# Optimization experiments

Measured on AMD Instinct MI355X. Metric: run time of the kernel, lower is better.

Reference implementation:

```python
import jax, jax.numpy as jnp
import numpy as np

# Dims: L list entries, T hutch samples, D = output_dim*inducing_size, H = 16 hidden
L, T, D, H = 32, 64, 8192, 16


def setup_inputs() -> dict:
    key = jax.random.key(0)
    k = jax.random.split(key, 4)
    return {
        "u": jax.random.normal(k[0], (L, D), jnp.float32),
        "w": jax.random.normal(k[1], (L, T, D), jnp.float32),  # Hutchinson Gaussian probes
        "W1": jax.random.normal(k[2], (H, D), jnp.float32) / np.sqrt(D).astype(np.float32),
        "b1": jnp.zeros((H,), jnp.float32),
        "W2": jax.random.normal(k[3], (D, H), jnp.float32) / np.sqrt(H).astype(np.float32),
        "b2": jnp.zeros((D,), jnp.float32),
    }


def reference(u, w, W1, b1, W2, b2):
    # f = W2 tanh(W1 u + b1) + b2 ; Jacobian J = W2 diag(1 - h^2) W1
    h = jnp.tanh(u @ W1.T + b1)                 # [L, H]
    f = h @ W2.T + b2                           # [L, D]  (f_u_list stacked)
    s = 1.0 - h * h                             # tanh' at preactivation, [L, H]
    # u_grad = J^T w  computed without materializing J: W1^T diag(s) W2^T w
    v = jnp.einsum('ltd,dh->lth', w, W2)        # W2^T w, [L, T, H]
    v = v * s[:, None, :]                       # diag(s) applied
    g = jnp.einsum('lth,hd->ltd', v, W1)        # J^T w, [L, T, D]
    traces = jnp.sum(g * w, axis=-1)            # w^T J w, [L, T]
    # mean over hutch samples, then mean over list entries -> [1, 1] like torch.mm output
    trace_final_mean = jnp.mean(traces).reshape(1, 1)
    return f, trace_final_mean
```

## Files before the change

### kernel.cpp

```cpp
#include <hip/hip_runtime.h>

typedef __attribute__((ext_vector_type(8))) short bf16x8;
typedef __attribute__((ext_vector_type(4))) float f32x4;

namespace {
constexpr int L = 32, T = 64, D = 8192, H = 16;
constexpr int M = L * T;
constexpr int KP = 16;
constexpr int CHUNK = D / KP;

constexpr size_t WS_WH  = 0;
constexpr size_t WS_WL  = WS_WH + 32 * 8192 / 2;
constexpr size_t WS_PRE = WS_WL + 32 * 8192 / 2;
constexpr size_t WS_AC  = WS_PRE + 32 * 8 * 16;
}

__device__ inline void split1(float f, short& h, short& l) {
  unsigned b = __float_as_uint(f);
  h = (short)(b >> 16);
  float lf = f - __uint_as_float(b & 0xFFFF0000u);
  l = (short)(__float_as_uint(lf) >> 16);
}

__device__ inline void split8(float4 a0, float4 a1, bf16x8& h, bf16x8& l) {
  float f[8] = {a0.x, a0.y, a0.z, a0.w, a1.x, a1.y, a1.z, a1.w};
#pragma unroll
  for (int i = 0; i < 8; ++i) {
    short hh, ll;
    split1(f[i], hh, ll);
    h[i] = hh; l[i] = ll;
  }
}

__global__ void k_prep_wcat(const float* __restrict__ W1,
                            const float* __restrict__ W2,
                            ushort* __restrict__ wh, ushort* __restrict__ wl,
                            float* __restrict__ ac, float* __restrict__ out) {
  int b = blockIdx.x, tid = threadIdx.x;
  if (b == 0 && tid == 0) out[(size_t)L * D] = 0.f;
  if (b < 32) {
    int d = b * 256 + tid;
    const float4* src = reinterpret_cast<const float4*>(W2 + (size_t)d * 16);
    float4 q0 = src[0], q1 = src[1], q2 = src[2], q3 = src[3];
    float v[16] = {q0.x, q0.y, q0.z, q0.w, q1.x, q1.y, q1.z, q1.w,
                   q2.x, q2.y, q2.z, q2.w, q3.x, q3.y, q3.z, q3.w};
#pragma unroll
    for (int c = 0; c < 16; ++c) {
      short hh, ll;
      split1(v[c], hh, ll);
      wh[(size_t)c * D + d] = (ushort)hh;
      wl[(size_t)c * D + d] = (ushort)ll;
    }
  } else if (b < 64) {
    int q = (b - 32) * 256 + tid;
#pragma unroll
    for (int j = 0; j < 4; ++j) {
      int idx = (q + j * 8192) * 4;
      float4 qv = *reinterpret_cast<const float4*>(W1 + idx);
      short h0, l0, h1, l1, h2, l2, h3, l3;
      split1(qv.x, h0, l0); split1(qv.y, h1, l1);
      split1(qv.z, h2, l2); split1(qv.w, h3, l3);
      ushort4 vh = {(ushort)h0, (ushort)h1, (ushort)h2, (ushort)h3};
      ushort4 vl = {(ushort)l0, (ushort)l1, (ushort)l2, (ushort)l3};
      *reinterpret_cast<ushort4*>(wh + (size_t)16 * D + idx) = vh;
      *reinterpret_cast<ushort4*>(wl + (size_t)16 * D + idx) = vl;
    }
  } else {
    int t = (b - 64) * 256 + tid;
    float4 z = {0.f, 0.f, 0.f, 0.f};
    float4* dst = reinterpret_cast<float4*>(ac);
#pragma unroll
    for (int j = 0; j < 4; ++j) dst[t + j * 4096] = z;
  }
}

__global__ void k_preact(const float* __restrict__ u,
                         const float* __restrict__ W1,
                         float* __restrict__ pre_partial) {
  int kc = blockIdx.x, l = blockIdx.y, tid = threadIdx.x;
  int d = kc * 1024 + tid * 4;
  float4 uv = *reinterpret_cast<const float4*>(u + (size_t)l * D + d);
  float acc[16];
#pragma unroll
  for (int h = 0; h < 16; ++h) {
    float4 wv = *reinterpret_cast<const float4*>(W1 + (size_t)h * D + d);
    float t = fmaf(uv.x, wv.x, 0.f);
    t = fmaf(uv.y, wv.y, t);
    t = fmaf(uv.z, wv.z, t);
    acc[h] = fmaf(uv.w, wv.w, t);
  }
#pragma unroll
  for (int h = 0; h < 16; ++h)
    for (int off = 1; off < 64; off <<= 1) acc[h] += __shfl_xor(acc[h], off);
  __shared__ float red[4][16];
  int lane = tid & 63, wv_ = tid >> 6;
  if (lane == 0) {
#pragma unroll
    for (int h = 0; h < 16; ++h) red[wv_][h] = acc[h];
  }
  __syncthreads();
  if (tid < 16)
    pre_partial[((size_t)l * 8 + kc) * 16 + tid] =
        red[0][tid] + red[1][tid] + red[2][tid] + red[3][tid];
}

__global__ void k_f(const float* __restrict__ pre_partial,
                    const float* __restrict__ b1,
                    const float* __restrict__ W2,
                    const float* __restrict__ b2,
                    float* __restrict__ fout) {
  __shared__ float hl[8][16];
  int tid = threadIdx.x;
  int lg = blockIdx.y;
  if (tid < 128) {
    int ll = tid >> 4, h = tid & 15, l = lg * 8 + ll;
    float p = b1[h];
#pragma unroll
    for (int kc = 0; kc < 8; ++kc) p += pre_partial[((size_t)l * 8 + kc) * 16 + h];
    hl[ll][h] = tanhf(p);
  }
  __syncthreads();
  int d = blockIdx.x * 256 + tid;
  const float4* w2r = reinterpret_cast<const float4*>(W2 + (size_t)d * 16);
  float4 q0 = w2r[0], q1 = w2r[1], q2 = w2r[2], q3 = w2r[3];
  float w2v[16] = {q0.x, q0.y, q0.z, q0.w, q1.x, q1.y, q1.z, q1.w,
                   q2.x, q2.y, q2.z, q2.w, q3.x, q3.y, q3.z, q3.w};
  float bv = b2[d];
#pragma unroll
  for (int ll = 0; ll < 8; ++ll) {
    float fv = bv;
#pragma unroll
    for (int h = 0; h < 16; ++h) fv = fmaf(hl[ll][h], w2v[h], fv);
    fout[(size_t)(lg * 8 + ll) * D + d] = fv;
  }
}

__global__ __launch_bounds__(256) void k_trace_ac(
    const float* __restrict__ w,
    const ushort* __restrict__ wh, const ushort* __restrict__ wl,
    float* __restrict__ ac) {
  int tid = threadIdx.x;
  int wave = tid >> 6, lane = tid & 63;
  int lrow = lane & 15, kg = lane >> 4;
  int kp = blockIdx.x;
  int rt = blockIdx.y * 4 + wave;
  int m0 = rt * 16;
  int k0 = kp * CHUNK;

  const float*  wrow = w  + (size_t)(m0 + lrow) * D + k0 + kg * 8;
  const ushort* bh0  = wh + (size_t)lrow * D + k0 + kg * 8;
  const ushort* bl0  = wl + (size_t)lrow * D + k0 + kg * 8;
  const ushort* bh1  = bh0 + (size_t)16 * D;
  const ushort* bl1  = bl0 + (size_t)16 * D;

  f32x4 acc0 = {0.f, 0.f, 0.f, 0.f};
  f32x4 acc1 = {0.f, 0.f, 0.f, 0.f};

  for (int kk = 0; kk < CHUNK / 32; ++kk) {
    int off = kk * 32;
    float4 a0 = *reinterpret_cast<const float4*>(wrow + off);
    float4 a1 = *reinterpret_cast<const float4*>(wrow + off + 4);
    bf16x8 ah, al;
    split8(a0, a1, ah, al);
    bf16x8 vbh0 = *reinterpret_cast<const bf16x8*>(bh0 + off);
    bf16x8 vbl0 = *reinterpret_cast<const bf16x8*>(bl0 + off);
    bf16x8 vbh1 = *reinterpret_cast<const bf16x8*>(bh1 + off);
    bf16x8 vbl1 = *reinterpret_cast<const bf16x8*>(bl1 + off);
    acc0 = __builtin_amdgcn_mfma_f32_16x16x32_bf16(ah, vbh0, acc0, 0, 0, 0);
    acc0 = __builtin_amdgcn_mfma_f32_16x16x32_bf16(ah, vbl0, acc0, 0, 0, 0);
    acc0 = __builtin_amdgcn_mfma_f32_16x16x32_bf16(al, vbh0, acc0, 0, 0, 0);
    acc1 = __builtin_amdgcn_mfma_f32_16x16x32_bf16(ah, vbh1, acc1, 0, 0, 0);
    acc1 = __builtin_amdgcn_mfma_f32_16x16x32_bf16(ah, vbl1, acc1, 0, 0, 0);
    acc1 = __builtin_amdgcn_mfma_f32_16x16x32_bf16(al, vbh1, acc1, 0, 0, 0);
  }

  float* dst = ac + (size_t)(m0 + kg * 4) * 32;
#pragma unroll
  for (int j = 0; j < 4; ++j) {
    atomicAdd(dst + (size_t)j * 32 + lrow,      acc0[j]);
    atomicAdd(dst + (size_t)j * 32 + 16 + lrow, acc1[j]);
  }
}

__global__ void k_trace_red(const float* __restrict__ ac,
                            const float* __restrict__ pre_partial,
                            const float* __restrict__ b1,
                            float* __restrict__ out) {
  __shared__ float s[16];
  int tid = threadIdx.x;
  int l = blockIdx.x;
  int m = l * 64 + tid;
  if (tid < 16) {
    float p = b1[tid];
#pragma unroll
    for (int kc = 0; kc < 8; ++kc) p += pre_partial[((size_t)l * 8 + kc) * 16 + tid];
    float t = tanhf(p);
    s[tid] = 1.f - t * t;
  }
  __syncthreads();
  const float4* src = reinterpret_cast<const float4*>(ac + (size_t)m * 32);
  float av[16], cv[16];
#pragma unroll
  for (int j = 0; j < 4; ++j) {
    float4 q = src[j];
    av[j * 4 + 0] = q.x; av[j * 4 + 1] = q.y;
    av[j * 4 + 2] = q.z; av[j * 4 + 3] = q.w;
  }
#pragma unroll
  for (int j = 0; j < 4; ++j) {
    float4 q = src[4 + j];
    cv[j * 4 + 0] = q.x; cv[j * 4 + 1] = q.y;
    cv[j * 4 + 2] = q.z; cv[j * 4 + 3] = q.w;
  }
  float tr = 0.f;
#pragma unroll
  for (int h = 0; h < 16; ++h) tr = fmaf(s[h] * av[h], cv[h], tr);
  for (int off = 1; off < 64; off <<= 1) tr += __shfl_xor(tr, off);
  if (tid == 0) atomicAdd(out + (size_t)L * D, tr * (1.0f / (float)(L * T)));
}

extern "C" void kernel_launch(void* const* d_in, const int* in_sizes, int n_in,
                              void* d_out, int out_size, void* d_ws, size_t ws_size,
                              hipStream_t stream) {
  const float* u  = (const float*)d_in[0];
  const float* w  = (const float*)d_in[1];
  const float* W1 = (const float*)d_in[2];
  const float* b1 = (const float*)d_in[3];
  const float* W2 = (const float*)d_in[4];
  const float* b2 = (const float*)d_in[5];
  float* out = (float*)d_out;
  float* ws  = (float*)d_ws;
  ushort* wcat_h = (ushort*)(ws + WS_WH);
  ushort* wcat_l = (ushort*)(ws + WS_WL);
  float* pre = ws + WS_PRE;
  float* acb = ws + WS_AC;

  hipLaunchKernelGGL(k_prep_wcat, dim3(80), dim3(256), 0, stream, W1, W2, wcat_h, wcat_l, acb, out);
  hipLaunchKernelGGL(k_preact,    dim3(8, 32), dim3(256), 0, stream, u, W1, pre);
  hipLaunchKernelGGL(k_f,         dim3(32, 4), dim3(256), 0, stream, pre, b1, W2, b2, out);
  hipLaunchKernelGGL(k_trace_ac,  dim3(KP, 32), dim3(256), 0, stream, w, wcat_h, wcat_l, acb);
  hipLaunchKernelGGL(k_trace_red, dim3(32), dim3(64), 0, stream, acb, pre, b1, out);
}
```

Measured before the change: 132.4 us.

## Merge five launches into three and double K-split of trace kernel

Folds the preactivation partials into the weight-prep kernel and merges the f computation with the trace reduction into a single tail kernel, cutting the launch count from five to three. The trace MFMA kernel now splits K into 32 chunks instead of 16 and its inner loop is fully unrolled, giving twice as many blocks to hide memory latency. In exchange there are twice as many atomic adds into the accumulator buffer. The f output is now computed after the trace kernel rather than before it.

```diff
diff --git a/kernel.cpp b/kernel.cpp
--- a/kernel.cpp
+++ b/kernel.cpp
@@ -6,7 +6,7 @@
 namespace {
 constexpr int L = 32, T = 64, D = 8192, H = 16;
 constexpr int M = L * T;
-constexpr int KP = 16;
+constexpr int KP = 32;
 constexpr int CHUNK = D / KP;
 
 constexpr size_t WS_WH  = 0;
@@ -32,10 +32,12 @@
   }
 }
 
-__global__ void k_prep_wcat(const float* __restrict__ W1,
-                            const float* __restrict__ W2,
-                            ushort* __restrict__ wh, ushort* __restrict__ wl,
-                            float* __restrict__ ac, float* __restrict__ out) {
+__global__ __launch_bounds__(256) void k_setup(
+    const float* __restrict__ u, const float* __restrict__ W1,
+    const float* __restrict__ W2,
+    ushort* __restrict__ wh, ushort* __restrict__ wl,
+    float* __restrict__ pre, float* __restrict__ ac,
+    float* __restrict__ out) {
   int b = blockIdx.x, tid = threadIdx.x;
   if (b == 0 && tid == 0) out[(size_t)L * D] = 0.f;
   if (b < 32) {
@@ -65,73 +67,39 @@
       *reinterpret_cast<ushort4*>(wh + (size_t)16 * D + idx) = vh;
       *reinterpret_cast<ushort4*>(wl + (size_t)16 * D + idx) = vl;
     }
-  } else {
+  } else if (b < 80) {
     int t = (b - 64) * 256 + tid;
     float4 z = {0.f, 0.f, 0.f, 0.f};
     float4* dst = reinterpret_cast<float4*>(ac);
 #pragma unroll
     for (int j = 0; j < 4; ++j) dst[t + j * 4096] = z;
-  }
-}
-
-__global__ void k_preact(const float* __restrict__ u,
-                         const float* __restrict__ W1,
-                         float* __restrict__ pre_partial) {
-  int kc = blockIdx.x, l = blockIdx.y, tid = threadIdx.x;
-  int d = kc * 1024 + tid * 4;
-  float4 uv = *reinterpret_cast<const float4*>(u + (size_t)l * D + d);
-  float acc[16];
-#pragma unroll
-  for (int h = 0; h < 16; ++h) {
-    float4 wv = *reinterpret_cast<const float4*>(W1 + (size_t)h * D + d);
-    float t = fmaf(uv.x, wv.x, 0.f);
-    t = fmaf(uv.y, wv.y, t);
-    t = fmaf(uv.z, wv.z, t);
-    acc[h] = fmaf(uv.w, wv.w, t);
-  }
-#pragma unroll
-  for (int h = 0; h < 16; ++h)
-    for (int off = 1; off < 64; off <<= 1) acc[h] += __shfl_xor(acc[h], off);
-  __shared__ float red[4][16];
-  int lane = tid & 63, wv_ = tid >> 6;
-  if (lane == 0) {
-#pragma unroll
-    for (int h = 0; h < 16; ++h) red[wv_][h] = acc[h];
-  }
-  __syncthreads();
-  if (tid < 16)
-    pre_partial[((size_t)l * 8 + kc) * 16 + tid] =
-        red[0][tid] + red[1][tid] + red[2][tid] + red[3][tid];
-}
-
-__global__ void k_f(const float* __restrict__ pre_partial,
-                    const float* __restrict__ b1,
-                    const float* __restrict__ W2,
-                    const float* __restrict__ b2,
-                    float* __restrict__ fout) {
-  __shared__ float hl[8][16];
-  int tid = threadIdx.x;
-  int lg = blockIdx.y;
-  if (tid < 128) {
-    int ll = tid >> 4, h = tid & 15, l = lg * 8 + ll;
-    float p = b1[h];
-#pragma unroll
-    for (int kc = 0; kc < 8; ++kc) p += pre_partial[((size_t)l * 8 + kc) * 16 + h];
-    hl[ll][h] = tanhf(p);
-  }
-  __syncthreads();
-  int d = blockIdx.x * 256 + tid;
-  const float4* w2r = reinterpret_cast<const float4*>(W2 + (size_t)d * 16);
-  float4 q0 = w2r[0], q1 = w2r[1], q2 = w2r[2], q3 = w2r[3];
-  float w2v[16] = {q0.x, q0.y, q0.z, q0.w, q1.x, q1.y, q1.z, q1.w,
-                   q2.x, q2.y, q2.z, q2.w, q3.x, q3.y, q3.z, q3.w};
-  float bv = b2[d];
-#pragma unroll
-  for (int ll = 0; ll < 8; ++ll) {
-    float fv = bv;
-#pragma unroll
-    for (int h = 0; h < 16; ++h) fv = fmaf(hl[ll][h], w2v[h], fv);
-    fout[(size_t)(lg * 8 + ll) * D + d] = fv;
+  } else {
+    int bb = b - 80;
+    int kc = bb & 7, l = bb >> 3;
+    int d = kc * 1024 + tid * 4;
+    float4 uv = *reinterpret_cast<const float4*>(u + (size_t)l * D + d);
+    float acc[16];
+#pragma unroll
+    for (int h = 0; h < 16; ++h) {
+      float4 wv = *reinterpret_cast<const float4*>(W1 + (size_t)h * D + d);
+      float t = fmaf(uv.x, wv.x, 0.f);
+      t = fmaf(uv.y, wv.y, t);
+      t = fmaf(uv.z, wv.z, t);
+      acc[h] = fmaf(uv.w, wv.w, t);
+    }
+#pragma unroll
+    for (int h = 0; h < 16; ++h)
+      for (int off = 1; off < 64; off <<= 1) acc[h] += __shfl_xor(acc[h], off);
+    __shared__ float red[4][16];
+    int lane = tid & 63, wv_ = tid >> 6;
+    if (lane == 0) {
+#pragma unroll
+      for (int h = 0; h < 16; ++h) red[wv_][h] = acc[h];
+    }
+    __syncthreads();
+    if (tid < 16)
+      pre[((size_t)l * 8 + kc) * 16 + tid] =
+          red[0][tid] + red[1][tid] + red[2][tid] + red[3][tid];
   }
 }
 
@@ -156,6 +124,7 @@
   f32x4 acc0 = {0.f, 0.f, 0.f, 0.f};
   f32x4 acc1 = {0.f, 0.f, 0.f, 0.f};
 
+#pragma unroll
   for (int kk = 0; kk < CHUNK / 32; ++kk) {
     int off = kk * 32;
     float4 a0 = *reinterpret_cast<const float4*>(wrow + off);
@@ -182,41 +151,69 @@
   }
 }
 
-__global__ void k_trace_red(const float* __restrict__ ac,
-                            const float* __restrict__ pre_partial,
-                            const float* __restrict__ b1,
-                            float* __restrict__ out) {
-  __shared__ float s[16];
-  int tid = threadIdx.x;
-  int l = blockIdx.x;
-  int m = l * 64 + tid;
-  if (tid < 16) {
-    float p = b1[tid];
-#pragma unroll
-    for (int kc = 0; kc < 8; ++kc) p += pre_partial[((size_t)l * 8 + kc) * 16 + tid];
-    float t = tanhf(p);
-    s[tid] = 1.f - t * t;
+__global__ __launch_bounds__(256) void k_tail(
+    const float* __restrict__ pre, const float* __restrict__ b1,
+    const float* __restrict__ W2, const float* __restrict__ b2,
+    const float* __restrict__ ac, float* __restrict__ out) {
+  int b = blockIdx.x, tid = threadIdx.x;
+  if (b >= 128) {
+    __shared__ float s[16];
+    int l = b - 128;
+    if (tid < 16) {
+      float p = b1[tid];
+#pragma unroll
+      for (int kc = 0; kc < 8; ++kc) p += pre[((size_t)l * 8 + kc) * 16 + tid];
+      float t = tanhf(p);
+      s[tid] = 1.f - t * t;
+    }
+    __syncthreads();
+    if (tid < 64) {
+      int m = l * 64 + tid;
+      const float4* src = reinterpret_cast<const float4*>(ac + (size_t)m * 32);
+      float av[16], cv[16];
+#pragma unroll
+      for (int j = 0; j < 4; ++j) {
+        float4 q = src[j];
+        av[j * 4 + 0] = q.x; av[j * 4 + 1] = q.y;
+        av[j * 4 + 2] = q.z; av[j * 4 + 3] = q.w;
+      }
+#pragma unroll
+      for (int j = 0; j < 4; ++j) {
+        float4 q = src[4 + j];
+        cv[j * 4 + 0] = q.x; cv[j * 4 + 1] = q.y;
+        cv[j * 4 + 2] = q.z; cv[j * 4 + 3] = q.w;
+      }
+      float tr = 0.f;
+#pragma unroll
+      for (int h = 0; h < 16; ++h) tr = fmaf(s[h] * av[h], cv[h], tr);
+      for (int off = 1; off < 64; off <<= 1) tr += __shfl_xor(tr, off);
+      if (tid == 0) atomicAdd(out + (size_t)L * D, tr * (1.0f / (float)(L * T)));
+    }
+    return;
+  }
+  __shared__ float hl[8][16];
+  int lg = b >> 5;
+  if (tid < 128) {
+    int ll = tid >> 4, h = tid & 15, l = lg * 8 + ll;
+    float p = b1[h];
+#pragma unroll
+    for (int kc = 0; kc < 8; ++kc) p += pre[((size_t)l * 8 + kc) * 16 + h];
+    hl[ll][h] = tanhf(p);
   }
   __syncthreads();
-  const float4* src = reinterpret_cast<const float4*>(ac + (size_t)m * 32);
-  float av[16], cv[16];
-#pragma unroll
-  for (int j = 0; j < 4; ++j) {
-    float4 q = src[j];
-    av[j * 4 + 0] = q.x; av[j * 4 + 1] = q.y;
-    av[j * 4 + 2] = q.z; av[j * 4 + 3] = q.w;
-  }
-#pragma unroll
-  for (int j = 0; j < 4; ++j) {
-    float4 q = src[4 + j];
-    cv[j * 4 + 0] = q.x; cv[j * 4 + 1] = q.y;
-    cv[j * 4 + 2] = q.z; cv[j * 4 + 3] = q.w;
-  }
-  float tr = 0.f;
-#pragma unroll
-  for (int h = 0; h < 16; ++h) tr = fmaf(s[h] * av[h], cv[h], tr);
-  for (int off = 1; off < 64; off <<= 1) tr += __shfl_xor(tr, off);
-  if (tid == 0) atomicAdd(out + (size_t)L * D, tr * (1.0f / (float)(L * T)));
+  int d = (b & 31) * 256 + tid;
+  const float4* w2r = reinterpret_cast<const float4*>(W2 + (size_t)d * 16);
+  float4 q0 = w2r[0], q1 = w2r[1], q2 = w2r[2], q3 = w2r[3];
+  float w2v[16] = {q0.x, q0.y, q0.z, q0.w, q1.x, q1.y, q1.z, q1.w,
+                   q2.x, q2.y, q2.z, q2.w, q3.x, q3.y, q3.z, q3.w};
+  float bv = b2[d];
+#pragma unroll
+  for (int ll = 0; ll < 8; ++ll) {
+    float fv = bv;
+#pragma unroll
+    for (int h = 0; h < 16; ++h) fv = fmaf(hl[ll][h], w2v[h], fv);
+    out[(size_t)(lg * 8 + ll) * D + d] = fv;
+  }
 }
 
 extern "C" void kernel_launch(void* const* d_in, const int* in_sizes, int n_in,
@@ -235,9 +232,10 @@
   float* pre = ws + WS_PRE;
   float* acb = ws + WS_AC;
 
-  hipLaunchKernelGGL(k_prep_wcat, dim3(80), dim3(256), 0, stream, W1, W2, wcat_h, wcat_l, acb, out);
-  hipLaunchKernelGGL(k_preact,    dim3(8, 32), dim3(256), 0, stream, u, W1, pre);
-  hipLaunchKernelGGL(k_f,         dim3(32, 4), dim3(256), 0, stream, pre, b1, W2, b2, out);
-  hipLaunchKernelGGL(k_trace_ac,  dim3(KP, 32), dim3(256), 0, stream, w, wcat_h, wcat_l, acb);
-  hipLaunchKernelGGL(k_trace_red, dim3(32), dim3(64), 0, stream, acb, pre, b1, out);
-}
+  hipLaunchKernelGGL(k_setup,    dim3(336), dim3(256), 0, stream,
+                     u, W1, W2, wcat_h, wcat_l, pre, acb, out);
+  hipLaunchKernelGGL(k_trace_ac, dim3(KP, 32), dim3(256), 0, stream,
+                     w, wcat_h, wcat_l, acb);
+  hipLaunchKernelGGL(k_tail,     dim3(160), dim3(256), 0, stream,
+                     pre, b1, W2, b2, acb, out);
+}
```

New measurement: 123.5 us. 1.07x faster.
